# Kernel tuning notes

Measured on AMD Instinct MI355X. Metric: run time of the kernel, lower is better.

The kernel has to match this reference:

```python
import jax, jax.numpy as jnp
import numpy as np

# ---- MERU-style Lorentz geometry helpers (space components, implicit time) ----

def _time(x, curv):
    # x: [..., D] space component; time = sqrt(1/curv + ||x||^2)
    return jnp.sqrt(1.0 / curv + jnp.sum(x * x, axis=-1))


def pairwise_dist(x, y, curv, eps=1e-8):
    # Lorentzian inner product for all pairs: <x,y>_L = x.y - x_t*y_t  -> [N, M]
    xt = _time(x, curv)
    yt = _time(y, curv)
    inner = jnp.einsum('nd,md->nm', x, y) - xt[:, None] * yt[None, :]
    c_xyl = -curv * inner  # >= 1 on the hyperboloid
    return jnp.arccosh(jnp.clip(c_xyl, 1.0 + eps, None)) / jnp.sqrt(curv)


def oxy_angle(x, y, curv, eps=1e-8):
    # exterior angle at x of geodesic triangle (origin, x, y); elementwise over batch
    xt = _time(x, curv)
    yt = _time(y, curv)
    c_xyl = curv * (jnp.sum(x * y, axis=-1) - xt * yt)  # <= -1
    acos_numer = yt + c_xyl * xt
    acos_denom = jnp.linalg.norm(x, axis=-1) * jnp.sqrt(jnp.clip(c_xyl * c_xyl - 1.0, 0.0, None))
    acos_input = acos_numer / (acos_denom + eps)
    return jnp.arccos(jnp.clip(acos_input, -1.0 + eps, 1.0 - eps))


def half_aperture(x, curv, min_radius=0.1, eps=1e-6):
    asin_input = 2.0 * min_radius / (jnp.linalg.norm(x, axis=-1) * jnp.sqrt(curv) + eps)
    return jnp.arcsin(jnp.clip(asin_input, -1.0 + eps, 1.0 - eps))


def soft_cross_entropy(logits, target_probs):
    # torch.nn.CrossEntropyLoss with probability targets (rows need not sum to 1)
    return jnp.mean(-jnp.sum(target_probs * jax.nn.log_softmax(logits, axis=-1), axis=-1))


def entailment_loss(fa, fb, curv, eps=1e-6):
    ang = oxy_angle(fa, fb, curv)
    ap = half_aperture(fa, curv, eps=eps)
    return jnp.mean(jnp.clip(ang - ap, 0.0, None))


def setup_inputs() -> dict:
    key = jax.random.key(0)
    k1, k2, k3, k4 = jax.random.split(key, 4)
    B, D = 4096, 512
    return {
        'image_features': jax.random.normal(k1, (B, D), dtype=jnp.float32),
        'dna_features': jax.random.normal(k2, (B, D), dtype=jnp.float32),
        'text_features': jax.random.normal(k3, (B, D), dtype=jnp.float32),
        'labels': jax.random.randint(k4, (B,), 0, 500, dtype=jnp.int64),
        'logit_scale': jnp.float32(10.0),
        'curv': jnp.float32(1.0),
    }


ENTAIL_WEIGHT = 0.2


def reference(image_features, dna_features, text_features, labels, logit_scale, curv):
    # world_size == 1: gathered features == local features
    label_mat = (labels[None, :] == labels[:, None]).astype(jnp.float32)  # [B, B]

    feats = [image_features, dna_features, text_features]  # idx 0=image, 1=dna, 2=text

    contrastive_losses = []
    entail_losses = []
    for ia in range(3):
        for ib in range(3):
            if ia == ib:
                continue
            sim_ab = -pairwise_dist(feats[ia], feats[ib], curv)
            sim_ba = -pairwise_dist(feats[ib], feats[ia], curv)
            contrastive_losses.append(soft_cross_entropy(logit_scale * sim_ab, label_mat))
            contrastive_losses.append(soft_cross_entropy(logit_scale * sim_ba, label_mat))
            # 2D features branch: entailment only for (dna, image) ordering
            if ia == 1 and ib == 0:
                entail_losses.append(entailment_loss(feats[1], feats[0], curv, eps=1e-6))
            elif ia == 0 and ib == 1:
                entail_losses.append(entailment_loss(feats[1], feats[0], curv, eps=1e-6))

    contrastive_total = sum(contrastive_losses) / len(contrastive_losses)
    entail_total = sum(entail_losses) / len(entail_losses)
    total = contrastive_total + ENTAIL_WEIGHT * entail_total
    return total, contrastive_total, entail_total
```

## Files before the change

kernel.cpp:

```cpp
#include <hip/hip_runtime.h>
#include <stdint.h>

#define B_SZ 4096
#define D_SZ 512
#define SHIFT 64.0f

typedef __attribute__((ext_vector_type(4))) float floatx4;
typedef __attribute__((ext_vector_type(2))) long lng2;
typedef unsigned char u8;
typedef unsigned int u32;

#define GLD_LDS16(gp, sp)                                                              \
    __builtin_amdgcn_global_load_lds(                                                  \
        (const __attribute__((address_space(1))) void*)(gp),                           \
        (__attribute__((address_space(3))) void*)(sp), 16, 0, 0)

#define FP8MFMA(accv, av, bv)                                                          \
    accv = __builtin_amdgcn_mfma_f32_16x16x32_fp8_fp8(av, bv, accv, 0, 0, 0)

__global__ __launch_bounds__(256) void prep_kernel(
    const float* __restrict__ img, const float* __restrict__ dna,
    const float* __restrict__ txt, const float* __restrict__ curv_p,
    const int* __restrict__ labels, int* __restrict__ hist,
    u8* __restrict__ f8, float* __restrict__ times,
    float* __restrict__ zero_f, float* __restrict__ ent_partial) {
    __shared__ int lhist[512];
    __shared__ float red[4];
    int t = threadIdx.x;
    int gid = blockIdx.x * 256 + t;
    if (gid < 49155) zero_f[gid] = 0.0f;

    if (blockIdx.x == 0) {
        lhist[t] = 0; lhist[t + 256] = 0;
        __syncthreads();
        for (int n = t; n < B_SZ; n += 256) atomicAdd(&lhist[labels[n]], 1);
        __syncthreads();
        hist[t] = lhist[t]; hist[t + 256] = lhist[t + 256];
    }

    int wave = gid >> 6;
    int lane = t & 63;
    const float* src = (wave < B_SZ) ? img : (wave < 2 * B_SZ) ? dna : txt;
    int row = wave & (B_SZ - 1);
    const float* p = src + row * D_SZ + lane * 8;
    float4 v0 = *(const float4*)(p);
    float4 v1 = *(const float4*)(p + 4);
    float ss = v0.x*v0.x + v0.y*v0.y + v0.z*v0.z + v0.w*v0.w
             + v1.x*v1.x + v1.y*v1.y + v1.z*v1.z + v1.w*v1.w;
    u32 w0 = __builtin_amdgcn_cvt_pk_fp8_f32(v0.x, v0.y, 0, false);
    w0 = __builtin_amdgcn_cvt_pk_fp8_f32(v0.z, v0.w, w0, true);
    u32 w1 = __builtin_amdgcn_cvt_pk_fp8_f32(v1.x, v1.y, 0, false);
    w1 = __builtin_amdgcn_cvt_pk_fp8_f32(v1.z, v1.w, w1, true);
    uint2 pk; pk.x = w0; pk.y = w1;
    int gperm = (lane & 56) | ((lane & 3) << 1) | ((lane >> 2) & 1);
    *(uint2*)(f8 + (size_t)wave * D_SZ + gperm * 8) = pk;

    bool isdna = (wave >= B_SZ) && (wave < 2 * B_SZ);
    float dot = 0.0f, ssy = 0.0f;
    if (isdna) {
        const float* y = img + row * D_SZ + lane * 8;
        float4 y0 = *(const float4*)y, y1 = *(const float4*)(y + 4);
        dot = v0.x*y0.x + v0.y*y0.y + v0.z*y0.z + v0.w*y0.w
            + v1.x*y1.x + v1.y*y1.y + v1.z*y1.z + v1.w*y1.w;
        ssy = y0.x*y0.x + y0.y*y0.y + y0.z*y0.z + y0.w*y0.w
            + y1.x*y1.x + y1.y*y1.y + y1.z*y1.z + y1.w*y1.w;
    }
    #pragma unroll
    for (int m = 1; m < 64; m <<= 1) {
        ss += __shfl_xor(ss, m);
        if (isdna) { dot += __shfl_xor(dot, m); ssy += __shfl_xor(ssy, m); }
    }
    float curv = curv_p[0];
    float ep = 0.0f;
    if (lane == 0) {
        float xt = sqrtf(1.0f / curv + ss);
        times[wave] = xt;
        if (isdna) {
            float yt = sqrtf(1.0f / curv + ssy);
            float nx = sqrtf(ss);
            float c = curv * (dot - xt * yt);
            float numer = yt + c * xt;
            float denom = nx * sqrtf(fmaxf(c * c - 1.0f, 0.0f));
            float ai = numer / (denom + 1e-8f);
            ai = fminf(fmaxf(ai, -1.0f + 1e-8f), 1.0f - 1e-8f);
            float ang = acosf(ai);
            float as_in = 0.2f / (nx * sqrtf(curv) + 1e-6f);
            as_in = fminf(fmaxf(as_in, -1.0f + 1e-6f), 1.0f - 1e-6f);
            float ap = asinf(as_in);
            ep = fmaxf(ang - ap, 0.0f);
        }
    }
    if (blockIdx.x >= 1024 && blockIdx.x < 2048) {
        if (lane == 0) red[t >> 6] = ep;
        __syncthreads();
        if (t == 0) ent_partial[blockIdx.x - 1024] = red[0] + red[1] + red[2] + red[3];
    }
}

__global__ __launch_bounds__(512, 4) void gemm_epi_kernel(
    const u8* __restrict__ f8, const float* __restrict__ times,
    const int* __restrict__ labels,
    const float* __restrict__ ls_p, const float* __restrict__ curv_p,
    float* __restrict__ rsum_e, float* __restrict__ rsum_t,
    float* __restrict__ csum_e, float* __restrict__ csum_t) {
    __shared__ u8 sA[3][128 * 64];
    __shared__ u8 sB[3][128 * 64];

    int z = blockIdx.z;
    int pa = (z == 2) ? 1 : 0;
    int pb = (z == 0) ? 1 : 2;
    const u8* A  = f8 + (size_t)pa * (B_SZ * D_SZ);
    const u8* Bm = f8 + (size_t)pb * (B_SZ * D_SZ);

    int t = threadIdx.x;
    int rowBlk = blockIdx.y * 128;
    int colBlk = blockIdx.x * 128;
    int wave = t >> 6, lane = t & 63;
    int wr = wave >> 1;
    int wc = wave & 1;

    int chunk = (t & 3) ^ ((t >> 3) & 3);
    const u8* gA = A  + (size_t)(rowBlk + (t >> 2)) * D_SZ + chunk * 16;
    const u8* gB = Bm + (size_t)(colBlk + (t >> 2)) * D_SZ + chunk * 16;

    int q = lane >> 4, s = lane & 15;
    int slot16 = (q ^ ((s >> 1) & 3)) << 4;
    int aBase = (wr * 32 + s) * 64 + slot16;
    int bBase = (wc * 64 + s) * 64 + slot16;

    floatx4 acc[2][4];
    #pragma unroll
    for (int ii = 0; ii < 2; ++ii)
        #pragma unroll
        for (int j = 0; j < 4; ++j) acc[ii][j] = (floatx4){0.f, 0.f, 0.f, 0.f};

    {
        GLD_LDS16(gA,      &sA[0][wave * 1024]);
        GLD_LDS16(gB,      &sB[0][wave * 1024]);
        GLD_LDS16(gA + 64, &sA[1][wave * 1024]);
        GLD_LDS16(gB + 64, &sB[1][wave * 1024]);
    }

    #pragma unroll
    for (int si = 0; si < D_SZ / 64; ++si) {
        const int cur = si % 3;
        asm volatile("s_waitcnt lgkmcnt(0)" ::: "memory");
        if (si < 7) { asm volatile("s_waitcnt vmcnt(2)" ::: "memory"); }
        else        { asm volatile("s_waitcnt vmcnt(0)" ::: "memory"); }
        asm volatile("s_barrier" ::: "memory");
        if (si < 6) {
            const int nxb = (si + 2) % 3;
            const int ko  = (si + 2) * 64;
            GLD_LDS16(gA + ko, &sA[nxb][wave * 1024]);
            GLD_LDS16(gB + ko, &sB[nxb][wave * 1024]);
        }
        const u8* pA = &sA[cur][0];
        const u8* pB = &sB[cur][0];
        lng2 a0 = *(const lng2*)(pA + aBase);
        lng2 a1 = *(const lng2*)(pA + aBase + 1024);
        lng2 b0 = *(const lng2*)(pB + bBase);
        lng2 b1 = *(const lng2*)(pB + bBase + 1024);
        lng2 b2 = *(const lng2*)(pB + bBase + 2048);
        lng2 b3 = *(const lng2*)(pB + bBase + 3072);
        FP8MFMA(acc[0][0], a0.x, b0.x); FP8MFMA(acc[0][1], a0.x, b1.x);
        FP8MFMA(acc[0][2], a0.x, b2.x); FP8MFMA(acc[0][3], a0.x, b3.x);
        FP8MFMA(acc[1][0], a1.x, b0.x); FP8MFMA(acc[1][1], a1.x, b1.x);
        FP8MFMA(acc[1][2], a1.x, b2.x); FP8MFMA(acc[1][3], a1.x, b3.x);
        FP8MFMA(acc[0][0], a0.y, b0.y); FP8MFMA(acc[0][1], a0.y, b1.y);
        FP8MFMA(acc[0][2], a0.y, b2.y); FP8MFMA(acc[0][3], a0.y, b3.y);
        FP8MFMA(acc[1][0], a1.y, b0.y); FP8MFMA(acc[1][1], a1.y, b1.y);
        FP8MFMA(acc[1][2], a1.y, b2.y); FP8MFMA(acc[1][3], a1.y, b3.y);
    }

    float ls = ls_p[0];
    float curv = curv_p[0];
    float rsc = rsqrtf(curv);
    float c2 = -ls * rsc;
    float c1 = c2 * 0.69314718f;
    float sh2p = SHIFT * 1.44269504f + c2;
    const float* tA = times + pa * B_SZ;
    const float* tB = times + pb * B_SZ;

    int rowbase = rowBlk + wr * 32;
    int colbase = colBlk + wc * 64;

    float tb[4]; int lb[4]; int mcol[4];
    #pragma unroll
    for (int j = 0; j < 4; ++j) {
        mcol[j] = colbase + j * 16 + s;
        tb[j] = tB[mcol[j]];
        lb[j] = labels[mcol[j]];
    }
    float colE[4] = {0.f, 0.f, 0.f, 0.f}, colT[4] = {0.f, 0.f, 0.f, 0.f};

    float* rsE = rsum_e + z * B_SZ;
    float* rsT = rsum_t + z * B_SZ;
    float* csE = csum_e + z * B_SZ;
    float* csT = csum_t + z * B_SZ;

    #pragma unroll
    for (int ii = 0; ii < 2; ++ii) {
        int nb = rowbase + ii * 16 + q * 4;
        float cta[4]; int la[4];
        #pragma unroll
        for (int r = 0; r < 4; ++r) { cta[r] = curv * tA[nb + r]; la[r] = labels[nb + r]; }
        float re[4] = {0.f, 0.f, 0.f, 0.f}, rt[4] = {0.f, 0.f, 0.f, 0.f};
        #pragma unroll
        for (int j = 0; j < 4; ++j) {
            floatx4 a = acc[ii][j];
            #pragma unroll
            for (int r = 0; r < 4; ++r) {
                float zc = fmaf(-curv, a[r], cta[r] * tb[j]);
                zc = fmaxf(zc, 1.0f + 1e-8f);
                float lz = __log2f(zc);
                float e = __builtin_amdgcn_exp2f(fmaf(c2, lz, sh2p));
                float tl = (la[r] == lb[j]) ? fmaf(c1, lz, c1) : 0.0f;
                re[r] += e; rt[r] += tl;
                colE[j] += e; colT[j] += tl;
            }
        }
        #pragma unroll
        for (int r = 0; r < 4; ++r) {
            #pragma unroll
            for (int m = 1; m <= 8; m <<= 1) {
                re[r] += __shfl_xor(re[r], m);
                rt[r] += __shfl_xor(rt[r], m);
            }
        }
        #pragma unroll
        for (int r = 0; r < 4; ++r) {
            if (s == r) {
                atomicAdd(&rsE[nb + r], re[r]);
                atomicAdd(&rsT[nb + r], rt[r]);
            }
        }
    }
    #pragma unroll
    for (int j = 0; j < 4; ++j) {
        colE[j] += __shfl_xor(colE[j], 16); colE[j] += __shfl_xor(colE[j], 32);
        colT[j] += __shfl_xor(colT[j], 16); colT[j] += __shfl_xor(colT[j], 32);
        if (q == 0) {
            atomicAdd(&csE[mcol[j]], colE[j]);
            atomicAdd(&csT[mcol[j]], colT[j]);
        }
    }
}

__global__ __launch_bounds__(256) void finalize_kernel(
    const float* __restrict__ rsum_e, const float* __restrict__ rsum_t,
    const float* __restrict__ csum_e, const float* __restrict__ csum_t,
    const int* __restrict__ labels, const int* __restrict__ hist,
    const float* __restrict__ ent_partial,
    float* __restrict__ ce_acc, float* __restrict__ ent_acc,
    int* __restrict__ done, float* __restrict__ out) {
    __shared__ float red[4], red2[4];
    int b = blockIdx.x, tid = threadIdx.x;
    int n = b * 256 + tid;
    float Sn = (float)hist[labels[n]];
    float part = 0.0f;
    #pragma unroll
    for (int p = 0; p < 3; ++p) {
        part += Sn * (__logf(rsum_e[p * B_SZ + n]) - SHIFT) - rsum_t[p * B_SZ + n];
        part += Sn * (__logf(csum_e[p * B_SZ + n]) - SHIFT) - csum_t[p * B_SZ + n];
    }
    float ep = (b < 4) ? ent_partial[b * 256 + tid] : 0.0f;
    #pragma unroll
    for (int m = 1; m < 64; m <<= 1) {
        part += __shfl_xor(part, m);
        ep   += __shfl_xor(ep, m);
    }
    if ((tid & 63) == 0) { red[tid >> 6] = part; red2[tid >> 6] = ep; }
    __syncthreads();
    if (tid == 0) {
        atomicAdd(ce_acc, red[0] + red[1] + red[2] + red[3]);
        atomicAdd(ent_acc, red2[0] + red2[1] + red2[2] + red2[3]);
        __threadfence();
        if (atomicAdd(done, 1) == 15) {
            float ce = atomicAdd(ce_acc, 0.0f);
            float ent = atomicAdd(ent_acc, 0.0f);
            float contr = ce / (6.0f * (float)B_SZ);
            ent /= (float)B_SZ;
            out[0] = contr + 0.2f * ent;
            out[1] = contr;
            out[2] = ent;
        }
    }
}

extern "C" void kernel_launch(void* const* d_in, const int* in_sizes, int n_in,
                              void* d_out, int out_size, void* d_ws, size_t ws_size,
                              hipStream_t stream) {
    const float* img    = (const float*)d_in[0];
    const float* dna    = (const float*)d_in[1];
    const float* txt    = (const float*)d_in[2];
    const int*   labels = (const int*)d_in[3];
    const float* ls     = (const float*)d_in[4];
    const float* curv   = (const float*)d_in[5];

    char* ws = (char*)d_ws;
    u8*    f8     = (u8*)ws;
    float* times  = (float*)(ws + 6291456);
    float* rsum_e = (float*)(ws + 6340608);
    float* rsum_t = (float*)(ws + 6389760);
    float* csum_e = (float*)(ws + 6438912);
    float* csum_t = (float*)(ws + 6488064);
    float* ce_acc = (float*)(ws + 6537216);
    float* ent_acc= (float*)(ws + 6537220);
    int*   done   = (int*)  (ws + 6537224);
    float* ent_p  = (float*)(ws + 6537228);
    int*   hist   = (int*)  (ws + 6541324);

    prep_kernel<<<3072, 256, 0, stream>>>(img, dna, txt, curv, labels, hist,
                                          f8, times, rsum_e, ent_p);
    dim3 g(32, 32, 3);
    gemm_epi_kernel<<<g, 512, 0, stream>>>(f8, times, labels, ls, curv,
                                           rsum_e, rsum_t, csum_e, csum_t);
    finalize_kernel<<<16, 256, 0, stream>>>(rsum_e, rsum_t, csum_e, csum_t,
                                            labels, hist, ent_p,
                                            ce_acc, ent_acc, done, (float*)d_out);
}
```

Measured before the change: 164.1 us.

## Halve GEMM block to four waves each computing a 64x64 tile

The fused GEMM+epilogue kernel moves from 8 waves of 32x64 sub-tiles to 4 waves of 64x64 sub-tiles per 128x128 block. Each wave now issues twice the global-to-LDS loads and holds 16 accumulator tiles, so B fragments read from LDS are reused across four A fragments. The intent is to cut LDS read traffic and per-thread overhead relative to MFMA work. In exchange, per-wave register pressure rises, waves per block halve, and the launch-bounds occupancy hint is dropped, which may reduce latency hiding.

```diff
diff --git a/kernel.cpp b/kernel.cpp
--- a/kernel.cpp
+++ b/kernel.cpp
@@ -97,7 +97,7 @@
     }
 }
 
-__global__ __launch_bounds__(512, 4) void gemm_epi_kernel(
+__global__ __launch_bounds__(256) void gemm_epi_kernel(
     const u8* __restrict__ f8, const float* __restrict__ times,
     const int* __restrict__ labels,
     const float* __restrict__ ls_p, const float* __restrict__ curv_p,
@@ -119,45 +119,55 @@
     int wr = wave >> 1;
     int wc = wave & 1;
 
-    int chunk = (t & 3) ^ ((t >> 3) & 3);
-    const u8* gA = A  + (size_t)(rowBlk + (t >> 2)) * D_SZ + chunk * 16;
-    const u8* gB = Bm + (size_t)(colBlk + (t >> 2)) * D_SZ + chunk * 16;
+    int chunk = (lane & 3) ^ ((lane >> 3) & 3);
+    const u8* gA0 = A  + (size_t)(rowBlk + wave * 32 + (lane >> 2)) * D_SZ + chunk * 16;
+    const u8* gA1 = gA0 + 16 * D_SZ;
+    const u8* gB0 = Bm + (size_t)(colBlk + wave * 32 + (lane >> 2)) * D_SZ + chunk * 16;
+    const u8* gB1 = gB0 + 16 * D_SZ;
 
     int q = lane >> 4, s = lane & 15;
     int slot16 = (q ^ ((s >> 1) & 3)) << 4;
-    int aBase = (wr * 32 + s) * 64 + slot16;
+    int aBase = (wr * 64 + s) * 64 + slot16;
     int bBase = (wc * 64 + s) * 64 + slot16;
 
-    floatx4 acc[2][4];
-    #pragma unroll
-    for (int ii = 0; ii < 2; ++ii)
+    floatx4 acc[4][4];
+    #pragma unroll
+    for (int ii = 0; ii < 4; ++ii)
         #pragma unroll
         for (int j = 0; j < 4; ++j) acc[ii][j] = (floatx4){0.f, 0.f, 0.f, 0.f};
 
     {
-        GLD_LDS16(gA,      &sA[0][wave * 1024]);
-        GLD_LDS16(gB,      &sB[0][wave * 1024]);
-        GLD_LDS16(gA + 64, &sA[1][wave * 1024]);
-        GLD_LDS16(gB + 64, &sB[1][wave * 1024]);
+        GLD_LDS16(gA0,      &sA[0][wave * 2048]);
+        GLD_LDS16(gA1,      &sA[0][wave * 2048 + 1024]);
+        GLD_LDS16(gB0,      &sB[0][wave * 2048]);
+        GLD_LDS16(gB1,      &sB[0][wave * 2048 + 1024]);
+        GLD_LDS16(gA0 + 64, &sA[1][wave * 2048]);
+        GLD_LDS16(gA1 + 64, &sA[1][wave * 2048 + 1024]);
+        GLD_LDS16(gB0 + 64, &sB[1][wave * 2048]);
+        GLD_LDS16(gB1 + 64, &sB[1][wave * 2048 + 1024]);
     }
 
     #pragma unroll
     for (int si = 0; si < D_SZ / 64; ++si) {
         const int cur = si % 3;
         asm volatile("s_waitcnt lgkmcnt(0)" ::: "memory");
-        if (si < 7) { asm volatile("s_waitcnt vmcnt(2)" ::: "memory"); }
+        if (si < 7) { asm volatile("s_waitcnt vmcnt(4)" ::: "memory"); }
         else        { asm volatile("s_waitcnt vmcnt(0)" ::: "memory"); }
         asm volatile("s_barrier" ::: "memory");
         if (si < 6) {
             const int nxb = (si + 2) % 3;
             const int ko  = (si + 2) * 64;
-            GLD_LDS16(gA + ko, &sA[nxb][wave * 1024]);
-            GLD_LDS16(gB + ko, &sB[nxb][wave * 1024]);
+            GLD_LDS16(gA0 + ko, &sA[nxb][wave * 2048]);
+            GLD_LDS16(gA1 + ko, &sA[nxb][wave * 2048 + 1024]);
+            GLD_LDS16(gB0 + ko, &sB[nxb][wave * 2048]);
+            GLD_LDS16(gB1 + ko, &sB[nxb][wave * 2048 + 1024]);
         }
         const u8* pA = &sA[cur][0];
         const u8* pB = &sB[cur][0];
         lng2 a0 = *(const lng2*)(pA + aBase);
         lng2 a1 = *(const lng2*)(pA + aBase + 1024);
+        lng2 a2 = *(const lng2*)(pA + aBase + 2048);
+        lng2 a3 = *(const lng2*)(pA + aBase + 3072);
         lng2 b0 = *(const lng2*)(pB + bBase);
         lng2 b1 = *(const lng2*)(pB + bBase + 1024);
         lng2 b2 = *(const lng2*)(pB + bBase + 2048);
@@ -166,10 +176,18 @@
         FP8MFMA(acc[0][2], a0.x, b2.x); FP8MFMA(acc[0][3], a0.x, b3.x);
         FP8MFMA(acc[1][0], a1.x, b0.x); FP8MFMA(acc[1][1], a1.x, b1.x);
         FP8MFMA(acc[1][2], a1.x, b2.x); FP8MFMA(acc[1][3], a1.x, b3.x);
+        FP8MFMA(acc[2][0], a2.x, b0.x); FP8MFMA(acc[2][1], a2.x, b1.x);
+        FP8MFMA(acc[2][2], a2.x, b2.x); FP8MFMA(acc[2][3], a2.x, b3.x);
+        FP8MFMA(acc[3][0], a3.x, b0.x); FP8MFMA(acc[3][1], a3.x, b1.x);
+        FP8MFMA(acc[3][2], a3.x, b2.x); FP8MFMA(acc[3][3], a3.x, b3.x);
         FP8MFMA(acc[0][0], a0.y, b0.y); FP8MFMA(acc[0][1], a0.y, b1.y);
         FP8MFMA(acc[0][2], a0.y, b2.y); FP8MFMA(acc[0][3], a0.y, b3.y);
         FP8MFMA(acc[1][0], a1.y, b0.y); FP8MFMA(acc[1][1], a1.y, b1.y);
         FP8MFMA(acc[1][2], a1.y, b2.y); FP8MFMA(acc[1][3], a1.y, b3.y);
+        FP8MFMA(acc[2][0], a2.y, b0.y); FP8MFMA(acc[2][1], a2.y, b1.y);
+        FP8MFMA(acc[2][2], a2.y, b2.y); FP8MFMA(acc[2][3], a2.y, b3.y);
+        FP8MFMA(acc[3][0], a3.y, b0.y); FP8MFMA(acc[3][1], a3.y, b1.y);
+        FP8MFMA(acc[3][2], a3.y, b2.y); FP8MFMA(acc[3][3], a3.y, b3.y);
     }
 
     float ls = ls_p[0];
@@ -181,7 +199,7 @@
     const float* tA = times + pa * B_SZ;
     const float* tB = times + pb * B_SZ;
 
-    int rowbase = rowBlk + wr * 32;
+    int rowbase = rowBlk + wr * 64;
     int colbase = colBlk + wc * 64;
 
     float tb[4]; int lb[4]; int mcol[4];
@@ -199,7 +217,7 @@
     float* csT = csum_t + z * B_SZ;
 
     #pragma unroll
-    for (int ii = 0; ii < 2; ++ii) {
+    for (int ii = 0; ii < 4; ++ii) {
         int nb = rowbase + ii * 16 + q * 4;
         float cta[4]; int la[4];
         #pragma unroll
@@ -313,7 +331,7 @@
     prep_kernel<<<3072, 256, 0, stream>>>(img, dna, txt, curv, labels, hist,
                                           f8, times, rsum_e, ent_p);
     dim3 g(32, 32, 3);
-    gemm_epi_kernel<<<g, 512, 0, stream>>>(f8, times, labels, ls, curv,
+    gemm_epi_kernel<<<g, 256, 0, stream>>>(f8, times, labels, ls, curv,
                                            rsum_e, rsum_t, csum_e, csum_t);
     finalize_kernel<<<16, 256, 0, stream>>>(rsum_e, rsum_t, csum_e, csum_t,
                                             labels, hist, ent_p,
```

New measurement: 168.4 us. +2.6%, slower.

## Make GEMM kernel persistent over six tiles with cross-tile prefetch

Applied to the files above, without the earlier changes.

The grid shrinks to 512 blocks, each looping over six consecutive output tiles. The first K-stages of the next tile are prefetched into LDS during the last K-step and the epilogue of the current tile, hiding load latency. This trades away concurrent resident blocks per CU, which reduces latency hiding through occupancy, and assigns work statically.

```diff
diff --git a/kernel.cpp b/kernel.cpp
--- a/kernel.cpp
+++ b/kernel.cpp
@@ -106,71 +106,15 @@
     __shared__ u8 sA[3][128 * 64];
     __shared__ u8 sB[3][128 * 64];
 
-    int z = blockIdx.z;
-    int pa = (z == 2) ? 1 : 0;
-    int pb = (z == 0) ? 1 : 2;
-    const u8* A  = f8 + (size_t)pa * (B_SZ * D_SZ);
-    const u8* Bm = f8 + (size_t)pb * (B_SZ * D_SZ);
-
     int t = threadIdx.x;
-    int rowBlk = blockIdx.y * 128;
-    int colBlk = blockIdx.x * 128;
     int wave = t >> 6, lane = t & 63;
     int wr = wave >> 1;
     int wc = wave & 1;
-
     int chunk = (t & 3) ^ ((t >> 3) & 3);
-    const u8* gA = A  + (size_t)(rowBlk + (t >> 2)) * D_SZ + chunk * 16;
-    const u8* gB = Bm + (size_t)(colBlk + (t >> 2)) * D_SZ + chunk * 16;
-
     int q = lane >> 4, s = lane & 15;
     int slot16 = (q ^ ((s >> 1) & 3)) << 4;
     int aBase = (wr * 32 + s) * 64 + slot16;
     int bBase = (wc * 64 + s) * 64 + slot16;
-
-    floatx4 acc[2][4];
-    #pragma unroll
-    for (int ii = 0; ii < 2; ++ii)
-        #pragma unroll
-        for (int j = 0; j < 4; ++j) acc[ii][j] = (floatx4){0.f, 0.f, 0.f, 0.f};
-
-    {
-        GLD_LDS16(gA,      &sA[0][wave * 1024]);
-        GLD_LDS16(gB,      &sB[0][wave * 1024]);
-        GLD_LDS16(gA + 64, &sA[1][wave * 1024]);
-        GLD_LDS16(gB + 64, &sB[1][wave * 1024]);
-    }
-
-    #pragma unroll
-    for (int si = 0; si < D_SZ / 64; ++si) {
-        const int cur = si % 3;
-        asm volatile("s_waitcnt lgkmcnt(0)" ::: "memory");
-        if (si < 7) { asm volatile("s_waitcnt vmcnt(2)" ::: "memory"); }
-        else        { asm volatile("s_waitcnt vmcnt(0)" ::: "memory"); }
-        asm volatile("s_barrier" ::: "memory");
-        if (si < 6) {
-            const int nxb = (si + 2) % 3;
-            const int ko  = (si + 2) * 64;
-            GLD_LDS16(gA + ko, &sA[nxb][wave * 1024]);
-            GLD_LDS16(gB + ko, &sB[nxb][wave * 1024]);
-        }
-        const u8* pA = &sA[cur][0];
-        const u8* pB = &sB[cur][0];
-        lng2 a0 = *(const lng2*)(pA + aBase);
-        lng2 a1 = *(const lng2*)(pA + aBase + 1024);
-        lng2 b0 = *(const lng2*)(pB + bBase);
-        lng2 b1 = *(const lng2*)(pB + bBase + 1024);
-        lng2 b2 = *(const lng2*)(pB + bBase + 2048);
-        lng2 b3 = *(const lng2*)(pB + bBase + 3072);
-        FP8MFMA(acc[0][0], a0.x, b0.x); FP8MFMA(acc[0][1], a0.x, b1.x);
-        FP8MFMA(acc[0][2], a0.x, b2.x); FP8MFMA(acc[0][3], a0.x, b3.x);
-        FP8MFMA(acc[1][0], a1.x, b0.x); FP8MFMA(acc[1][1], a1.x, b1.x);
-        FP8MFMA(acc[1][2], a1.x, b2.x); FP8MFMA(acc[1][3], a1.x, b3.x);
-        FP8MFMA(acc[0][0], a0.y, b0.y); FP8MFMA(acc[0][1], a0.y, b1.y);
-        FP8MFMA(acc[0][2], a0.y, b2.y); FP8MFMA(acc[0][3], a0.y, b3.y);
-        FP8MFMA(acc[1][0], a1.y, b0.y); FP8MFMA(acc[1][1], a1.y, b1.y);
-        FP8MFMA(acc[1][2], a1.y, b2.y); FP8MFMA(acc[1][3], a1.y, b3.y);
-    }
 
     float ls = ls_p[0];
     float curv = curv_p[0];
@@ -178,70 +122,150 @@
     float c2 = -ls * rsc;
     float c1 = c2 * 0.69314718f;
     float sh2p = SHIFT * 1.44269504f + c2;
-    const float* tA = times + pa * B_SZ;
-    const float* tB = times + pb * B_SZ;
-
-    int rowbase = rowBlk + wr * 32;
-    int colbase = colBlk + wc * 64;
-
-    float tb[4]; int lb[4]; int mcol[4];
-    #pragma unroll
-    for (int j = 0; j < 4; ++j) {
-        mcol[j] = colbase + j * 16 + s;
-        tb[j] = tB[mcol[j]];
-        lb[j] = labels[mcol[j]];
-    }
-    float colE[4] = {0.f, 0.f, 0.f, 0.f}, colT[4] = {0.f, 0.f, 0.f, 0.f};
-
-    float* rsE = rsum_e + z * B_SZ;
-    float* rsT = rsum_t + z * B_SZ;
-    float* csE = csum_e + z * B_SZ;
-    float* csT = csum_t + z * B_SZ;
-
-    #pragma unroll
-    for (int ii = 0; ii < 2; ++ii) {
-        int nb = rowbase + ii * 16 + q * 4;
-        float cta[4]; int la[4];
-        #pragma unroll
-        for (int r = 0; r < 4; ++r) { cta[r] = curv * tA[nb + r]; la[r] = labels[nb + r]; }
-        float re[4] = {0.f, 0.f, 0.f, 0.f}, rt[4] = {0.f, 0.f, 0.f, 0.f};
+
+    const u8* gA = nullptr;  const u8* gB = nullptr;
+
+    #pragma unroll 1
+    for (int tile = 0; tile < 6; ++tile) {
+        int tl  = blockIdx.x * 6 + tile;
+        int z   = tl >> 10;
+        int rem = tl & 1023;
+        int rowBlk = (rem >> 5) * 128;
+        int colBlk = (rem & 31) * 128;
+        int pa = (z == 2) ? 1 : 0;
+        int pb = (z == 0) ? 1 : 2;
+        const u8* A  = f8 + (size_t)pa * (B_SZ * D_SZ);
+        const u8* Bm = f8 + (size_t)pb * (B_SZ * D_SZ);
+        const u8* gA_n = A  + (size_t)(rowBlk + (t >> 2)) * D_SZ + chunk * 16;
+        const u8* gB_n = Bm + (size_t)(colBlk + (t >> 2)) * D_SZ + chunk * 16;
+
+        if (tile == 0) {
+            GLD_LDS16(gA_n,      &sA[0][wave * 1024]);
+            GLD_LDS16(gB_n,      &sB[0][wave * 1024]);
+            GLD_LDS16(gA_n + 64, &sA[1][wave * 1024]);
+            GLD_LDS16(gB_n + 64, &sB[1][wave * 1024]);
+        }
+        gA = gA_n; gB = gB_n;
+
+        floatx4 acc[2][4];
+        #pragma unroll
+        for (int ii = 0; ii < 2; ++ii)
+            #pragma unroll
+            for (int j = 0; j < 4; ++j) acc[ii][j] = (floatx4){0.f, 0.f, 0.f, 0.f};
+
+        int tln  = tl + 1;
+        int zn   = tln >> 10;
+        int remn = tln & 1023;
+        const u8* An  = f8 + (size_t)((zn == 2) ? 1 : 0) * (B_SZ * D_SZ);
+        const u8* Bn  = f8 + (size_t)((zn == 0) ? 1 : 2) * (B_SZ * D_SZ);
+        const u8* gAx = An + (size_t)(((remn >> 5) * 128) + (t >> 2)) * D_SZ + chunk * 16;
+        const u8* gBx = Bn + (size_t)(((remn & 31) * 128) + (t >> 2)) * D_SZ + chunk * 16;
+
+        #pragma unroll
+        for (int si = 0; si < D_SZ / 64; ++si) {
+            const int cur = si % 3;
+            asm volatile("s_waitcnt lgkmcnt(0)" ::: "memory");
+            if (si < 7) { asm volatile("s_waitcnt vmcnt(2)" ::: "memory"); }
+            else        { asm volatile("s_waitcnt vmcnt(0)" ::: "memory"); }
+            asm volatile("s_barrier" ::: "memory");
+            if (si < 6) {
+                const int nxb = (si + 2) % 3;
+                const int ko  = (si + 2) * 64;
+                GLD_LDS16(gA + ko, &sA[nxb][wave * 1024]);
+                GLD_LDS16(gB + ko, &sB[nxb][wave * 1024]);
+            } else if (si == 7 && tile < 5) {
+                GLD_LDS16(gAx, &sA[0][wave * 1024]);
+                GLD_LDS16(gBx, &sB[0][wave * 1024]);
+            }
+            const u8* pA = &sA[cur][0];
+            const u8* pB = &sB[cur][0];
+            lng2 a0 = *(const lng2*)(pA + aBase);
+            lng2 a1 = *(const lng2*)(pA + aBase + 1024);
+            lng2 b0 = *(const lng2*)(pB + bBase);
+            lng2 b1 = *(const lng2*)(pB + bBase + 1024);
+            lng2 b2 = *(const lng2*)(pB + bBase + 2048);
+            lng2 b3 = *(const lng2*)(pB + bBase + 3072);
+            FP8MFMA(acc[0][0], a0.x, b0.x); FP8MFMA(acc[0][1], a0.x, b1.x);
+            FP8MFMA(acc[0][2], a0.x, b2.x); FP8MFMA(acc[0][3], a0.x, b3.x);
+            FP8MFMA(acc[1][0], a1.x, b0.x); FP8MFMA(acc[1][1], a1.x, b1.x);
+            FP8MFMA(acc[1][2], a1.x, b2.x); FP8MFMA(acc[1][3], a1.x, b3.x);
+            FP8MFMA(acc[0][0], a0.y, b0.y); FP8MFMA(acc[0][1], a0.y, b1.y);
+            FP8MFMA(acc[0][2], a0.y, b2.y); FP8MFMA(acc[0][3], a0.y, b3.y);
+            FP8MFMA(acc[1][0], a1.y, b0.y); FP8MFMA(acc[1][1], a1.y, b1.y);
+            FP8MFMA(acc[1][2], a1.y, b2.y); FP8MFMA(acc[1][3], a1.y, b3.y);
+        }
+
+        if (tile < 5) {
+            asm volatile("s_waitcnt lgkmcnt(0)" ::: "memory");
+            asm volatile("s_barrier" ::: "memory");
+            GLD_LDS16(gAx + 64, &sA[1][wave * 1024]);
+            GLD_LDS16(gBx + 64, &sB[1][wave * 1024]);
+        }
+
+        const float* tA = times + pa * B_SZ;
+        const float* tB = times + pb * B_SZ;
+        int rowbase = rowBlk + wr * 32;
+        int colbase = colBlk + wc * 64;
+
+        float tb[4]; int lb[4]; int mcol[4];
         #pragma unroll
         for (int j = 0; j < 4; ++j) {
-            floatx4 a = acc[ii][j];
+            mcol[j] = colbase + j * 16 + s;
+            tb[j] = tB[mcol[j]];
+            lb[j] = labels[mcol[j]];
+        }
+        float colE[4] = {0.f, 0.f, 0.f, 0.f}, colT[4] = {0.f, 0.f, 0.f, 0.f};
+
+        float* rsE = rsum_e + z * B_SZ;
+        float* rsT = rsum_t + z * B_SZ;
+        float* csE = csum_e + z * B_SZ;
+        float* csT = csum_t + z * B_SZ;
+
+        #pragma unroll
+        for (int ii = 0; ii < 2; ++ii) {
+            int nb = rowbase + ii * 16 + q * 4;
+            float cta[4]; int la[4];
+            #pragma unroll
+            for (int r = 0; r < 4; ++r) { cta[r] = curv * tA[nb + r]; la[r] = labels[nb + r]; }
+            float re[4] = {0.f, 0.f, 0.f, 0.f}, rt[4] = {0.f, 0.f, 0.f, 0.f};
+            #pragma unroll
+            for (int j = 0; j < 4; ++j) {
+                floatx4 a = acc[ii][j];
+                #pragma unroll
+                for (int r = 0; r < 4; ++r) {
+                    float zc = fmaf(-curv, a[r], cta[r] * tb[j]);
+                    zc = fmaxf(zc, 1.0f + 1e-8f);
+                    float lz = __log2f(zc);
+                    float e = __builtin_amdgcn_exp2f(fmaf(c2, lz, sh2p));
+                    float tl2 = (la[r] == lb[j]) ? fmaf(c1, lz, c1) : 0.0f;
+                    re[r] += e; rt[r] += tl2;
+                    colE[j] += e; colT[j] += tl2;
+                }
+            }
             #pragma unroll
             for (int r = 0; r < 4; ++r) {
-                float zc = fmaf(-curv, a[r], cta[r] * tb[j]);
-                zc = fmaxf(zc, 1.0f + 1e-8f);
-                float lz = __log2f(zc);
-                float e = __builtin_amdgcn_exp2f(fmaf(c2, lz, sh2p));
-                float tl = (la[r] == lb[j]) ? fmaf(c1, lz, c1) : 0.0f;
-                re[r] += e; rt[r] += tl;
-                colE[j] += e; colT[j] += tl;
-            }
-        }
-        #pragma unroll
-        for (int r = 0; r < 4; ++r) {
-            #pragma unroll
-            for (int m = 1; m <= 8; m <<= 1) {
-                re[r] += __shfl_xor(re[r], m);
-                rt[r] += __shfl_xor(rt[r], m);
-            }
-        }
-        #pragma unroll
-        for (int r = 0; r < 4; ++r) {
-            if (s == r) {
-                atomicAdd(&rsE[nb + r], re[r]);
-                atomicAdd(&rsT[nb + r], rt[r]);
-            }
-        }
-    }
-    #pragma unroll
-    for (int j = 0; j < 4; ++j) {
-        colE[j] += __shfl_xor(colE[j], 16); colE[j] += __shfl_xor(colE[j], 32);
-        colT[j] += __shfl_xor(colT[j], 16); colT[j] += __shfl_xor(colT[j], 32);
-        if (q == 0) {
-            atomicAdd(&csE[mcol[j]], colE[j]);
-            atomicAdd(&csT[mcol[j]], colT[j]);
+                #pragma unroll
+                for (int m = 1; m <= 8; m <<= 1) {
+                    re[r] += __shfl_xor(re[r], m);
+                    rt[r] += __shfl_xor(rt[r], m);
+                }
+            }
+            #pragma unroll
+            for (int r = 0; r < 4; ++r) {
+                if (s == r) {
+                    atomicAdd(&rsE[nb + r], re[r]);
+                    atomicAdd(&rsT[nb + r], rt[r]);
+                }
+            }
+        }
+        #pragma unroll
+        for (int j = 0; j < 4; ++j) {
+            colE[j] += __shfl_xor(colE[j], 16); colE[j] += __shfl_xor(colE[j], 32);
+            colT[j] += __shfl_xor(colT[j], 16); colT[j] += __shfl_xor(colT[j], 32);
+            if (q == 0) {
+                atomicAdd(&csE[mcol[j]], colE[j]);
+                atomicAdd(&csT[mcol[j]], colT[j]);
+            }
         }
     }
 }
@@ -312,9 +336,8 @@
 
     prep_kernel<<<3072, 256, 0, stream>>>(img, dna, txt, curv, labels, hist,
                                           f8, times, rsum_e, ent_p);
-    dim3 g(32, 32, 3);
-    gemm_epi_kernel<<<g, 512, 0, stream>>>(f8, times, labels, ls, curv,
-                                           rsum_e, rsum_t, csum_e, csum_t);
+    gemm_epi_kernel<<<512, 512, 0, stream>>>(f8, times, labels, ls, curv,
+                                             rsum_e, rsum_t, csum_e, csum_t);
     finalize_kernel<<<16, 256, 0, stream>>>(rsum_e, rsum_t, csum_e, csum_t,
                                             labels, hist, ent_p,
                                             ce_acc, ent_acc, done, (float*)d_out);
```

New measurement: 150.6 us (median of 2 runs). -8.3%, faster.
